# Kernel optimization log

Hardware: AMD Instinct MI355X
Metric: run time of the kernel (lower is better)

## Reference

```python
import jax, jax.numpy as jnp
import numpy as np

N_CHANNELS = 512
D_K = 64
N_HEADS = N_CHANNELS // D_K  # 8
SCALE = 1.0 / np.sqrt(np.sqrt(D_K))
EPS = 1e-8


def pixnorm(x, axis=-1):
    return x * jax.lax.rsqrt(jnp.mean(x * x, axis=axis, keepdims=True) + EPS)


def setup_inputs() -> dict:
    key = jax.random.key(0)
    k1, k2, k3 = jax.random.split(key, 3)
    x = jax.random.normal(k1, (16, N_CHANNELS, 32, 32), dtype=jnp.float32)
    # 1x1 conv weights (bias=False) stored as [out, in]
    w_proj = jax.random.normal(k2, (3 * N_CHANNELS, N_CHANNELS), dtype=jnp.float32) * (1.0 / np.sqrt(N_CHANNELS))
    w_out = jax.random.normal(k3, (N_CHANNELS, N_CHANNELS), dtype=jnp.float32) * (1.0 / np.sqrt(N_CHANNELS))
    return {"x": x, "w_proj": w_proj, "w_out": w_out}


def reference(x, w_proj, w_out):
    B, C, H, W = x.shape
    S = H * W
    # tokens: [B, S, C]
    xt = x.reshape(B, C, S).transpose(0, 2, 1)
    # 1x1 conv projection -> [B, S, 3C]
    h = jnp.einsum('bsc,oc->bso', xt, w_proj)
    qkv = h.reshape(B, S, N_HEADS, 3 * D_K)
    q, k, v = jnp.split(qkv, 3, axis=-1)  # each [B, S, H, d]
    q = pixnorm(q)
    k = pixnorm(k)
    v = pixnorm(v)
    attn = jnp.einsum('bihd,bjhd->bijh', q * SCALE, k * SCALE)
    attn = jax.nn.softmax(attn, axis=2)
    res = jnp.einsum('bijh,bjhd->bihd', attn, v)  # [B, S, H, d]
    res = res.reshape(B, S, C)
    res = jnp.einsum('bsc,oc->bso', res, w_out)
    res = res.transpose(0, 2, 1).reshape(B, C, H, W)
    return x + res
```

## Files before the change

kernel.cpp:

```cpp
#include <hip/hip_runtime.h>
#include <hip/hip_bf16.h>
#include <math.h>

typedef float f32x4 __attribute__((ext_vector_type(4)));
typedef __bf16 bf16x8 __attribute__((ext_vector_type(8)));
typedef __bf16 bf16x4 __attribute__((ext_vector_type(4)));
typedef unsigned u32x4 __attribute__((ext_vector_type(4)));

#define DEVFN static __device__ __forceinline__

DEVFN void gload16(const void* g, void* l) {
  __builtin_amdgcn_global_load_lds(
      (const __attribute__((address_space(1))) unsigned int*)g,
      (__attribute__((address_space(3))) unsigned int*)l, 16, 0, 0);
}

DEVFN f32x4 mfma16(bf16x8 a, bf16x8 b, f32x4 c) {
  return __builtin_amdgcn_mfma_f32_16x16x32_bf16(a, b, c, 0, 0, 0);
}

DEVFN unsigned cvtpk(float lo, float hi) {
  unsigned r;
  asm("v_cvt_pk_bf16_f32 %0, %1, %2" : "=v"(r) : "v"(lo), "v"(hi));
  return r;
}

#define WAITV4() asm volatile("s_waitcnt vmcnt(4)" ::: "memory")
#define WAITV0() asm volatile("s_waitcnt vmcnt(0)" ::: "memory")

__global__ __launch_bounds__(256) void cast_weights_k(
    const float* __restrict__ wp, const float* __restrict__ wo,
    __bf16* __restrict__ wpb, __bf16* __restrict__ wob) {
  int i = blockIdx.x * 256 + threadIdx.x;
  if (i < 1536 * 512) {
    wpb[i] = (__bf16)wp[i];
  } else {
    int j = i - 1536 * 512;
    wob[j] = (__bf16)wo[j];
  }
}

__global__ __launch_bounds__(256) void transpose_x_k(const float* __restrict__ x,
                                                     __bf16* __restrict__ xt) {
  __shared__ float tile[64][65];
  int b = blockIdx.z, c0 = blockIdx.y * 64, s0 = blockIdx.x * 64;
  int t = threadIdx.x;
  int r = t >> 2, q = (t & 3) << 4;
  const float* src = x + ((size_t)(b * 512 + c0 + r)) * 1024 + s0 + q;
#pragma unroll
  for (int i = 0; i < 4; i++) {
    float4 f = *reinterpret_cast<const float4*>(src + i * 4);
    tile[r][q + i * 4 + 0] = f.x;
    tile[r][q + i * 4 + 1] = f.y;
    tile[r][q + i * 4 + 2] = f.z;
    tile[r][q + i * 4 + 3] = f.w;
  }
  __syncthreads();
  bf16x8 o0, o1;
#pragma unroll
  for (int i = 0; i < 8; i++) o0[i] = (__bf16)tile[q + i][r];
#pragma unroll
  for (int i = 0; i < 8; i++) o1[i] = (__bf16)tile[q + 8 + i][r];
  __bf16* dst = xt + ((size_t)(b * 1024 + s0 + r)) * 512 + c0 + q;
  *reinterpret_cast<bf16x8*>(dst) = o0;
  *reinterpret_cast<bf16x8*>(dst + 8) = o1;
}

template <int MODE>
__global__ __launch_bounds__(256, 4) void gemm_bt_k(
    const __bf16* __restrict__ A, const __bf16* __restrict__ Bt,
    float* __restrict__ Cf, const float* __restrict__ Xres,
    __bf16* __restrict__ Qo, __bf16* __restrict__ Ko, __bf16* __restrict__ Vto) {
  __shared__ __attribute__((aligned(16))) char smem[32768];
  const int K = 512;
  int p = blockIdx.x, xcd = p & 7, idx = p >> 3;
  int m0, n0, z;
  if (MODE == 2) {
    m0 = (xcd * 16 + idx / 12) * 128;
    n0 = (idx % 12) * 128;
    z = 0;
  } else {
    z = xcd * 2 + idx / 32;
    int rem = idx % 32;
    m0 = (rem >> 3) * 128;
    n0 = (rem & 7) * 128;
    Bt += (size_t)z * (1024L * 512);
  }
  int tid = threadIdx.x, wave = tid >> 6, lane = tid & 63;
  int fr = lane & 15, fq = lane >> 4;
  int wm = (wave >> 1) * 64, wn = (wave & 1) * 64;
  f32x4 acc[4][4] = {};
  int offs[2], rr[2], scc[2];
#pragma unroll
  for (int i = 0; i < 2; i++) {
    offs[i] = wave * 2048 + i * 1024 + lane * 16;
    rr[i] = offs[i] >> 6;
    scc[i] = (offs[i] & 63) ^ (((rr[i] ^ (rr[i] >> 2)) & 3) << 4);
  }
  int rdsw = (fr ^ (fr >> 2)) & 3;
  const char* Ap = (const char*)A;
  const char* Bp = (const char*)Bt;

#define GSTAGE(k0_, buf_)                                                       \
  {                                                                             \
    char* as_ = smem + (buf_)*8192;                                             \
    char* bs_ = smem + 16384 + (buf_)*8192;                                     \
    _Pragma("unroll") for (int i = 0; i < 2; i++)                               \
        gload16(Ap + (size_t)(m0 + rr[i]) * 1024 + (k0_)*2 + scc[i],            \
                as_ + offs[i]);                                                 \
    _Pragma("unroll") for (int i = 0; i < 2; i++)                               \
        gload16(Bp + (size_t)(n0 + rr[i]) * 1024 + (k0_)*2 + scc[i],            \
                bs_ + offs[i]);                                                 \
  }

  GSTAGE(0, 0);
  GSTAGE(32, 1);
  int cur = 0;
  for (int k0 = 0; k0 < K; k0 += 32) {
    if (k0 + 32 < K) WAITV4(); else WAITV0();
    __builtin_amdgcn_s_barrier();
    __builtin_amdgcn_sched_barrier(0);
    const char* as = smem + cur * 8192;
    const char* bs = smem + 16384 + cur * 8192;
    bf16x8 af[4], bfr[4];
#pragma unroll
    for (int mi = 0; mi < 4; mi++)
      af[mi] = *reinterpret_cast<const bf16x8*>(
          as + (wm + mi * 16 + fr) * 64 + ((fq ^ rdsw) << 4));
#pragma unroll
    for (int ni = 0; ni < 4; ni++)
      bfr[ni] = *reinterpret_cast<const bf16x8*>(
          bs + (wn + ni * 16 + fr) * 64 + ((fq ^ rdsw) << 4));
    __builtin_amdgcn_s_setprio(1);
#pragma unroll
    for (int mi = 0; mi < 4; mi++)
#pragma unroll
      for (int ni = 0; ni < 4; ni++)
        acc[mi][ni] = mfma16(af[mi], bfr[ni], acc[mi][ni]);
    __builtin_amdgcn_s_setprio(0);
    __builtin_amdgcn_s_barrier();
    if (k0 + 64 < K) GSTAGE(k0 + 64, cur);
    cur ^= 1;
  }
#undef GSTAGE

  if (MODE == 1) {
    float* Co = Cf + (size_t)z * (512L * 1024);
    const float* Xr = Xres + (size_t)z * (512L * 1024);
#pragma unroll
    for (int mi = 0; mi < 4; mi++)
#pragma unroll
      for (int i = 0; i < 4; i++) {
        int row = m0 + wm + mi * 16 + fq * 4 + i;
#pragma unroll
        for (int ni = 0; ni < 4; ni++) {
          size_t idxo = (size_t)row * 1024 + n0 + wn + ni * 16 + fr;
          Co[idxo] = acc[mi][ni][i] + Xr[idxo];
        }
      }
  } else {
    int g0 = n0 + wn;
    int head = g0 / 192;
    int grp = (g0 >> 6) % 3;
    int b = m0 >> 10, sb = m0 & 1023;
    int bh = b * 8 + head;
    float nrm[4][4];
#pragma unroll
    for (int mi = 0; mi < 4; mi++)
#pragma unroll
      for (int i = 0; i < 4; i++) {
        float ss = 0.f;
#pragma unroll
        for (int ni = 0; ni < 4; ni++) ss += acc[mi][ni][i] * acc[mi][ni][i];
#pragma unroll
        for (int off = 1; off < 16; off <<= 1) ss += __shfl_xor(ss, off);
        float nv = rsqrtf(ss * (1.0f / 64.0f) + 1e-8f);
        if (grp == 0) nv *= 0.18033688011112042f;
        nrm[mi][i] = nv;
      }
    if (grp < 2) {
      __bf16* dst = (grp == 0 ? Qo : Ko) + (size_t)bh * 65536;
#pragma unroll
      for (int mi = 0; mi < 4; mi++)
#pragma unroll
        for (int i = 0; i < 4; i++) {
          int s = sb + wm + mi * 16 + fq * 4 + i;
#pragma unroll
          for (int ni = 0; ni < 4; ni++)
            dst[(size_t)s * 64 + ni * 16 + fr] = (__bf16)(acc[mi][ni][i] * nrm[mi][i]);
        }
    }
    __syncthreads();
    if (grp == 2) {
#pragma unroll
      for (int mi = 0; mi < 4; mi++)
#pragma unroll
        for (int i = 0; i < 4; i++) {
          int r = wm + mi * 16 + fq * 4 + i;
#pragma unroll
          for (int ni = 0; ni < 4; ni++) {
            int col2 = (2 * (ni * 16 + fr)) ^ ((r & 31) << 2);
            *(__bf16*)(smem + r * 128 + col2) = (__bf16)(acc[mi][ni][i] * nrm[mi][i]);
          }
        }
    }
    __syncthreads();
    if (grp == 2) {
      int sl = wm + lane;
      int l = sl & 63;
      int pl = ((l >> 2) & 3) * 16 + (l >> 4) * 4 + (l & 3);
      __bf16* vdst = Vto + (size_t)bh * 65536 + sb + (sl & 64) + pl;
#pragma unroll 8
      for (int d = 0; d < 64; d++) {
        __bf16 v = *(const __bf16*)(smem + sl * 128 + ((2 * d) ^ ((sl & 31) << 2)));
        vdst[(size_t)d * 1024] = v;
      }
    }
  }
}

__global__ __launch_bounds__(256, 4) void attn_k(const __bf16* __restrict__ Q,
                                                 const __bf16* __restrict__ Kb,
                                                 const __bf16* __restrict__ Vt,
                                                 __bf16* __restrict__ Res) {
  __shared__ __attribute__((aligned(16))) char lds[32768];
  int p = blockIdx.x;
  int v = (p & 7) * 128 + (p >> 3);
  int qt = v & 7, bh = v >> 3;
  int wave = threadIdx.x >> 6, lane = threadIdx.x & 63;
  int fr = lane & 15, fq = lane >> 4;
  const __bf16* Qb = Q + (size_t)bh * 65536;
  const char* Kbase = (const char*)(Kb + (size_t)bh * 65536);
  const char* Vbase = (const char*)(Vt + (size_t)bh * 65536);
  bf16x8 qf[2][2];
#pragma unroll
  for (int qs = 0; qs < 2; qs++)
#pragma unroll
    for (int kk = 0; kk < 2; kk++)
      qf[qs][kk] = *reinterpret_cast<const bf16x8*>(
          Qb + (size_t)(qt * 128 + qs * 64 + wave * 16 + fr) * 64 + kk * 32 + fq * 8);

  bf16x8 ones;
#pragma unroll
  for (int j = 0; j < 8; j++) ones[j] = (__bf16)1.0f;

  f32x4 oa[2][4] = {};
  f32x4 lacc[2] = {};

  int o0 = wave * 2048 + lane * 16;
  int o1 = o0 + 1024;
  int r0 = o0 >> 7, c0 = o0 & 127, r1 = o1 >> 7, c1 = o1 & 127;
  int s0 = c0 ^ ((r0 & 7) << 4), s1 = c1 ^ ((r1 & 7) << 4);
  int swr = (fr & 7) << 4;

#define STAGE(kt_, buf_)                                                        \
  {                                                                             \
    char* ks_ = lds + (buf_)*8192;                                              \
    char* vs_ = lds + 16384 + (buf_)*8192;                                      \
    gload16(Kbase + (size_t)(kt_)*8192 + r0 * 128 + s0, ks_ + o0);              \
    gload16(Kbase + (size_t)(kt_)*8192 + r1 * 128 + s1, ks_ + o1);              \
    gload16(Vbase + (size_t)r0 * 2048 + (kt_)*128 + s0, vs_ + o0);              \
    gload16(Vbase + (size_t)r1 * 2048 + (kt_)*128 + s1, vs_ + o1);              \
  }

#define QKT(buf_)                                                               \
  {                                                                             \
    const char* ksc_ = lds + (buf_)*8192;                                       \
    __builtin_amdgcn_s_setprio(1);                                              \
    _Pragma("unroll") for (int ni = 0; ni < 4; ni++) {                          \
      bf16x8 kf0 = *reinterpret_cast<const bf16x8*>(                            \
          ksc_ + (ni * 16 + fr) * 128 + ((fq * 16) ^ swr));                     \
      bf16x8 kf1 = *reinterpret_cast<const bf16x8*>(                            \
          ksc_ + (ni * 16 + fr) * 128 + ((64 + fq * 16) ^ swr));                \
      _Pragma("unroll") for (int qs = 0; qs < 2; qs++) {                        \
        sa[qs][ni] = mfma16(kf0, qf[qs][0], sa[qs][ni]);                        \
        sa[qs][ni] = mfma16(kf1, qf[qs][1], sa[qs][ni]);                        \
      }                                                                         \
    }                                                                           \
    __builtin_amdgcn_s_setprio(0);                                              \
  }

  STAGE(0, 0);
  STAGE(1, 1);
  WAITV4();
  __builtin_amdgcn_s_barrier();
  __builtin_amdgcn_sched_barrier(0);
  f32x4 sa[2][4] = {};
  QKT(0);
  for (int kt = 0; kt < 16; kt++) {
    int cur = kt & 1;
    const char* vsc = lds + 16384 + cur * 8192;
    bf16x8 pb[2][2];
#pragma unroll
    for (int qs = 0; qs < 2; qs++) {
#pragma unroll
      for (int ni = 0; ni < 4; ni++)
#pragma unroll
        for (int i = 0; i < 4; i++)
          sa[qs][ni][i] = __builtin_amdgcn_exp2f(sa[qs][ni][i]);
#pragma unroll
      for (int kk2 = 0; kk2 < 2; kk2++) {
        u32x4 u;
        u[0] = cvtpk(sa[qs][2 * kk2][0], sa[qs][2 * kk2][1]);
        u[1] = cvtpk(sa[qs][2 * kk2][2], sa[qs][2 * kk2][3]);
        u[2] = cvtpk(sa[qs][2 * kk2 + 1][0], sa[qs][2 * kk2 + 1][1]);
        u[3] = cvtpk(sa[qs][2 * kk2 + 1][2], sa[qs][2 * kk2 + 1][3]);
        pb[qs][kk2] = __builtin_bit_cast(bf16x8, u);
      }
      lacc[qs] = mfma16(ones, pb[qs][0], lacc[qs]);
      lacc[qs] = mfma16(ones, pb[qs][1], lacc[qs]);
    }
    __builtin_amdgcn_s_setprio(1);
#pragma unroll
    for (int nd = 0; nd < 4; nd++) {
      int vrow = (nd * 16 + fr) * 128;
#pragma unroll
      for (int kk2 = 0; kk2 < 2; kk2++) {
        bf16x8 vf = *reinterpret_cast<const bf16x8*>(
            vsc + vrow + ((fq * 32 + kk2 * 16) ^ swr));
#pragma unroll
        for (int qs = 0; qs < 2; qs++)
          oa[qs][nd] = mfma16(vf, pb[qs][kk2], oa[qs][nd]);
      }
    }
    __builtin_amdgcn_s_setprio(0);
    if (kt == 15) break;
    __builtin_amdgcn_s_barrier();
    if (kt + 2 < 16) {
      STAGE(kt + 2, cur);
      WAITV4();
    } else {
      WAITV0();
    }
    __builtin_amdgcn_s_barrier();
    __builtin_amdgcn_sched_barrier(0);
#pragma unroll
    for (int qs = 0; qs < 2; qs++)
#pragma unroll
      for (int ni = 0; ni < 4; ni++) sa[qs][ni] = (f32x4){0.f, 0.f, 0.f, 0.f};
    QKT(cur ^ 1);
  }
  int b = bh >> 3, hd = bh & 7;
#pragma unroll
  for (int qs = 0; qs < 2; qs++) {
    int q = qt * 128 + qs * 64 + wave * 16 + fr;
    float inv_l = 1.0f / lacc[qs][0];
    __bf16* dst = Res + ((size_t)(b * 1024 + q)) * 512 + hd * 64 + fq * 4;
#pragma unroll
    for (int nd = 0; nd < 4; nd++) {
      bf16x4 ov;
#pragma unroll
      for (int i = 0; i < 4; i++) ov[i] = (__bf16)(oa[qs][nd][i] * inv_l);
      *reinterpret_cast<bf16x4*>(dst + nd * 16) = ov;
    }
  }
#undef STAGE
#undef QKT
}

extern "C" void kernel_launch(void* const* d_in, const int* in_sizes, int n_in,
                              void* d_out, int out_size, void* d_ws, size_t ws_size,
                              hipStream_t stream) {
  const float* x = (const float*)d_in[0];
  const float* wp = (const float*)d_in[1];
  const float* wo = (const float*)d_in[2];
  float* out = (float*)d_out;
  char* w = (char*)d_ws;
  __bf16* wpb = (__bf16*)(w);
  __bf16* wob = (__bf16*)(w + 1572864);
  __bf16* xt = (__bf16*)(w + 2097152);
  __bf16* Qb = (__bf16*)(w + 18874368);
  __bf16* Kb = (__bf16*)(w + 35651584);
  __bf16* Vtb = (__bf16*)(w + 52428800);
  __bf16* resb = (__bf16*)(w + 69206016);

  cast_weights_k<<<4096, 256, 0, stream>>>(wp, wo, wpb, wob);
  transpose_x_k<<<dim3(16, 8, 16), 256, 0, stream>>>(x, xt);
  gemm_bt_k<2><<<1536, 256, 0, stream>>>(xt, wpb, nullptr, nullptr, Qb, Kb, Vtb);
  attn_k<<<1024, 256, 0, stream>>>(Qb, Kb, Vtb, resb);
  gemm_bt_k<1><<<512, 256, 0, stream>>>(wob, resb, out, x, nullptr, nullptr,
                                        nullptr);
}
```

Baseline: 118.7 us.

## Restructure GEMM to 256x64 tiles with LDS-resident B and register-streamed A

Changes GEMM block tiles from 128x128 to 256x64. The whole 64xK B slice is loaded into 64KB LDS once up front, and A fragments are read directly from global memory into registers with double buffering. This removes the per-k-step barriers and the LDS staging of A. In exchange, LDS use rises to 64KB per block, which reduces occupancy, and A is read straight from global/L2 without any staging. The V-transpose epilogue is adjusted so each block handles a single q/k/v group.

After: 154.6 us. 1.3x slower.

```diff
diff --git a/kernel.cpp b/kernel.cpp
--- a/kernel.cpp
+++ b/kernel.cpp
@@ -67,82 +67,67 @@
 }
 
 template <int MODE>
-__global__ __launch_bounds__(256, 4) void gemm_bt_k(
+__global__ __launch_bounds__(256) void gemm_bt_k(
     const __bf16* __restrict__ A, const __bf16* __restrict__ Bt,
     float* __restrict__ Cf, const float* __restrict__ Xres,
     __bf16* __restrict__ Qo, __bf16* __restrict__ Ko, __bf16* __restrict__ Vto) {
-  __shared__ __attribute__((aligned(16))) char smem[32768];
-  const int K = 512;
+  __shared__ __attribute__((aligned(16))) char smem[65536];
   int p = blockIdx.x, xcd = p & 7, idx = p >> 3;
   int m0, n0, z;
   if (MODE == 2) {
-    m0 = (xcd * 16 + idx / 12) * 128;
-    n0 = (idx % 12) * 128;
+    m0 = (xcd * 8 + idx / 24) * 256;
+    n0 = (idx % 24) * 64;
     z = 0;
   } else {
     z = xcd * 2 + idx / 32;
     int rem = idx % 32;
-    m0 = (rem >> 3) * 128;
-    n0 = (rem & 7) * 128;
+    m0 = (rem >> 4) * 256;
+    n0 = (rem & 15) * 64;
     Bt += (size_t)z * (1024L * 512);
   }
   int tid = threadIdx.x, wave = tid >> 6, lane = tid & 63;
   int fr = lane & 15, fq = lane >> 4;
-  int wm = (wave >> 1) * 64, wn = (wave & 1) * 64;
+
+  {
+    int srow = tid >> 2, sslot = tid & 3;
+    int ssw = (srow ^ (srow >> 2)) & 3;
+    const char* Bsrc = (const char*)Bt + (size_t)(n0 + srow) * 1024 +
+                       ((sslot ^ ssw) << 4);
+#pragma unroll
+    for (int j = 0; j < 16; j++)
+      gload16(Bsrc + j * 64, smem + j * 4096 + tid * 16);
+  }
+  __syncthreads();
+
+  const char* Abase = (const char*)A + (size_t)(m0 + wave * 64 + fr) * 1024 + fq * 16;
+  int rdsw4 = ((fr ^ (fr >> 2)) & 3) << 4;
   f32x4 acc[4][4] = {};
-  int offs[2], rr[2], scc[2];
-#pragma unroll
-  for (int i = 0; i < 2; i++) {
-    offs[i] = wave * 2048 + i * 1024 + lane * 16;
-    rr[i] = offs[i] >> 6;
-    scc[i] = (offs[i] & 63) ^ (((rr[i] ^ (rr[i] >> 2)) & 3) << 4);
-  }
-  int rdsw = (fr ^ (fr >> 2)) & 3;
-  const char* Ap = (const char*)A;
-  const char* Bp = (const char*)Bt;
-
-#define GSTAGE(k0_, buf_)                                                       \
-  {                                                                             \
-    char* as_ = smem + (buf_)*8192;                                             \
-    char* bs_ = smem + 16384 + (buf_)*8192;                                     \
-    _Pragma("unroll") for (int i = 0; i < 2; i++)                               \
-        gload16(Ap + (size_t)(m0 + rr[i]) * 1024 + (k0_)*2 + scc[i],            \
-                as_ + offs[i]);                                                 \
-    _Pragma("unroll") for (int i = 0; i < 2; i++)                               \
-        gload16(Bp + (size_t)(n0 + rr[i]) * 1024 + (k0_)*2 + scc[i],            \
-                bs_ + offs[i]);                                                 \
-  }
-
-  GSTAGE(0, 0);
-  GSTAGE(32, 1);
-  int cur = 0;
-  for (int k0 = 0; k0 < K; k0 += 32) {
-    if (k0 + 32 < K) WAITV4(); else WAITV0();
-    __builtin_amdgcn_s_barrier();
-    __builtin_amdgcn_sched_barrier(0);
-    const char* as = smem + cur * 8192;
-    const char* bs = smem + 16384 + cur * 8192;
-    bf16x8 af[4], bfr[4];
-#pragma unroll
-    for (int mi = 0; mi < 4; mi++)
-      af[mi] = *reinterpret_cast<const bf16x8*>(
-          as + (wm + mi * 16 + fr) * 64 + ((fq ^ rdsw) << 4));
+  bf16x8 af[2][4];
+#pragma unroll
+  for (int mi = 0; mi < 4; mi++)
+    af[0][mi] = *reinterpret_cast<const bf16x8*>(Abase + mi * 16384);
+
+#pragma unroll
+  for (int kt = 0; kt < 16; kt++) {
+    if (kt + 1 < 16) {
+#pragma unroll
+      for (int mi = 0; mi < 4; mi++)
+        af[(kt + 1) & 1][mi] = *reinterpret_cast<const bf16x8*>(
+            Abase + mi * 16384 + (kt + 1) * 64);
+    }
+    bf16x8 bfr[4];
 #pragma unroll
     for (int ni = 0; ni < 4; ni++)
       bfr[ni] = *reinterpret_cast<const bf16x8*>(
-          bs + (wn + ni * 16 + fr) * 64 + ((fq ^ rdsw) << 4));
+          smem + kt * 4096 + (ni * 16 + fr) * 64 + ((fq << 4) ^ rdsw4));
     __builtin_amdgcn_s_setprio(1);
 #pragma unroll
     for (int mi = 0; mi < 4; mi++)
 #pragma unroll
       for (int ni = 0; ni < 4; ni++)
-        acc[mi][ni] = mfma16(af[mi], bfr[ni], acc[mi][ni]);
+        acc[mi][ni] = mfma16(af[kt & 1][mi], bfr[ni], acc[mi][ni]);
     __builtin_amdgcn_s_setprio(0);
-    __builtin_amdgcn_s_barrier();
-    if (k0 + 64 < K) GSTAGE(k0 + 64, cur);
-    cur ^= 1;
-  }
-#undef GSTAGE
+  }
 
   if (MODE == 1) {
     float* Co = Cf + (size_t)z * (512L * 1024);
@@ -151,17 +136,16 @@
     for (int mi = 0; mi < 4; mi++)
 #pragma unroll
       for (int i = 0; i < 4; i++) {
-        int row = m0 + wm + mi * 16 + fq * 4 + i;
+        int row = m0 + wave * 64 + mi * 16 + fq * 4 + i;
 #pragma unroll
         for (int ni = 0; ni < 4; ni++) {
-          size_t idxo = (size_t)row * 1024 + n0 + wn + ni * 16 + fr;
+          size_t idxo = (size_t)row * 1024 + n0 + ni * 16 + fr;
           Co[idxo] = acc[mi][ni][i] + Xr[idxo];
         }
       }
   } else {
-    int g0 = n0 + wn;
-    int head = g0 / 192;
-    int grp = (g0 >> 6) % 3;
+    int head = n0 / 192;
+    int grp = (n0 >> 6) % 3;
     int b = m0 >> 10, sb = m0 & 1023;
     int bh = b * 8 + head;
     float nrm[4][4];
@@ -184,36 +168,32 @@
       for (int mi = 0; mi < 4; mi++)
 #pragma unroll
         for (int i = 0; i < 4; i++) {
-          int s = sb + wm + mi * 16 + fq * 4 + i;
+          int s = sb + wave * 64 + mi * 16 + fq * 4 + i;
 #pragma unroll
           for (int ni = 0; ni < 4; ni++)
             dst[(size_t)s * 64 + ni * 16 + fr] = (__bf16)(acc[mi][ni][i] * nrm[mi][i]);
         }
-    }
-    __syncthreads();
-    if (grp == 2) {
+    } else {
+      __syncthreads();
 #pragma unroll
       for (int mi = 0; mi < 4; mi++)
 #pragma unroll
         for (int i = 0; i < 4; i++) {
-          int r = wm + mi * 16 + fq * 4 + i;
+          int r = wave * 64 + mi * 16 + fq * 4 + i;
 #pragma unroll
           for (int ni = 0; ni < 4; ni++) {
             int col2 = (2 * (ni * 16 + fr)) ^ ((r & 31) << 2);
             *(__bf16*)(smem + r * 128 + col2) = (__bf16)(acc[mi][ni][i] * nrm[mi][i]);
           }
         }
-    }
-    __syncthreads();
-    if (grp == 2) {
-      int sl = wm + lane;
-      int l = sl & 63;
+      __syncthreads();
+      int l = tid & 63;
       int pl = ((l >> 2) & 3) * 16 + (l >> 4) * 4 + (l & 3);
-      __bf16* vdst = Vto + (size_t)bh * 65536 + sb + (sl & 64) + pl;
+      __bf16* vdst = Vto + (size_t)bh * 65536 + sb + (tid & 192) + pl;
 #pragma unroll 8
       for (int d = 0; d < 64; d++) {
-        __bf16 v = *(const __bf16*)(smem + sl * 128 + ((2 * d) ^ ((sl & 31) << 2)));
-        vdst[(size_t)d * 1024] = v;
+        __bf16 vv = *(const __bf16*)(smem + tid * 128 + ((2 * d) ^ ((tid & 31) << 2)));
+        vdst[(size_t)d * 1024] = vv;
       }
     }
   }
```

## Use 256x256-tile 512-thread QKV projection GEMM with 128-deep K stages

Applied to the files above, without the earlier changes.

Splits the templated GEMM into a dedicated QKV projection kernel and an output-projection kernel. The QKV kernel uses 256x256 output tiles, 8 waves and 128-wide K stages double-buffered in 128KB of LDS, which cuts the number of global loads per FLOP and the number of barriers. This trades occupancy (one block per CU, 384 blocks on 256 CUs) and much higher register pressure for better data reuse. The pixnorm and V-transpose epilogue is adapted to per-wave 128x64 tiles.

New measurement: 129.1 us. 8.8% more time.

```diff
diff --git a/kernel.cpp b/kernel.cpp
--- a/kernel.cpp
+++ b/kernel.cpp
@@ -25,6 +25,7 @@
   return r;
 }
 
+#define WAITV8() asm volatile("s_waitcnt vmcnt(8)" ::: "memory")
 #define WAITV4() asm volatile("s_waitcnt vmcnt(4)" ::: "memory")
 #define WAITV0() asm volatile("s_waitcnt vmcnt(0)" ::: "memory")
 
@@ -66,26 +67,165 @@
   *reinterpret_cast<bf16x8*>(dst + 8) = o1;
 }
 
-template <int MODE>
-__global__ __launch_bounds__(256, 4) void gemm_bt_k(
+__global__ __launch_bounds__(512) void gemm_qkv_k(
     const __bf16* __restrict__ A, const __bf16* __restrict__ Bt,
-    float* __restrict__ Cf, const float* __restrict__ Xres,
     __bf16* __restrict__ Qo, __bf16* __restrict__ Ko, __bf16* __restrict__ Vto) {
+  __shared__ __attribute__((aligned(16))) char smem[131072];
+  int p = blockIdx.x, xcd = p & 7, idx = p >> 3;
+  int m0 = (xcd * 8 + idx / 6) * 256;
+  int n0 = (idx % 6) * 256;
+  int tid = threadIdx.x, wave = tid >> 6, lane = tid & 63;
+  int fr = lane & 15, fq = lane >> 4;
+  int wr = wave >> 2, wc = wave & 3;
+  const char* Ap = (const char*)A;
+  const char* Bp = (const char*)Bt;
+  int so[2], srow[2], ssw[2];
+#pragma unroll
+  for (int j = 0; j < 2; j++) {
+    so[j] = j * 8192 + tid * 16;
+    srow[j] = so[j] >> 7;
+    ssw[j] = (so[j] & 127) ^ ((srow[j] & 7) << 4);
+  }
+  int swr = (fr & 7) << 4;
+
+#define GSTAGE(kt_, buf_)                                                       \
+  {                                                                             \
+    char* ab_ = smem + (buf_)*32768;                                            \
+    char* bb_ = smem + 65536 + (buf_)*32768;                                    \
+    _Pragma("unroll") for (int h = 0; h < 2; h++)                               \
+        _Pragma("unroll") for (int j = 0; j < 2; j++) {                         \
+      gload16(Ap + (size_t)(m0 + h * 128 + srow[j]) * 1024 + (kt_)*128 + ssw[j],\
+              ab_ + h * 16384 + so[j]);                                         \
+      gload16(Bp + (size_t)(n0 + h * 128 + srow[j]) * 1024 + (kt_)*128 + ssw[j],\
+              bb_ + h * 16384 + so[j]);                                         \
+    }                                                                           \
+  }
+
+  f32x4 acc[8][4] = {};
+  GSTAGE(0, 0);
+  GSTAGE(1, 1);
+#pragma unroll
+  for (int kt = 0; kt < 8; kt++) {
+    if (kt < 7) WAITV8(); else WAITV0();
+    __builtin_amdgcn_s_barrier();
+    __builtin_amdgcn_sched_barrier(0);
+    const char* ab = smem + (kt & 1) * 32768 + wr * 16384;
+    const char* bb = smem + 65536 + (kt & 1) * 32768;
+#pragma unroll
+    for (int mh = 0; mh < 2; mh++) {
+      bf16x8 af[4][2];
+#pragma unroll
+      for (int m4 = 0; m4 < 4; m4++) {
+        int rloc = (mh * 4 + m4) * 16 + fr;
+#pragma unroll
+        for (int kk = 0; kk < 2; kk++)
+          af[m4][kk] = *reinterpret_cast<const bf16x8*>(
+              ab + rloc * 128 + ((kk * 64 + fq * 16) ^ swr));
+      }
+#pragma unroll
+      for (int nh = 0; nh < 2; nh++) {
+        bf16x8 bfr[2][2];
+#pragma unroll
+        for (int n2 = 0; n2 < 2; n2++) {
+          int rn = wc * 64 + (nh * 2 + n2) * 16 + fr;
+#pragma unroll
+          for (int kk = 0; kk < 2; kk++)
+            bfr[n2][kk] = *reinterpret_cast<const bf16x8*>(
+                bb + (rn >> 7) * 16384 + (rn & 127) * 128 +
+                ((kk * 64 + fq * 16) ^ swr));
+        }
+        __builtin_amdgcn_s_setprio(1);
+#pragma unroll
+        for (int m4 = 0; m4 < 4; m4++)
+#pragma unroll
+          for (int n2 = 0; n2 < 2; n2++)
+#pragma unroll
+            for (int kk = 0; kk < 2; kk++)
+              acc[mh * 4 + m4][nh * 2 + n2] =
+                  mfma16(af[m4][kk], bfr[n2][kk], acc[mh * 4 + m4][nh * 2 + n2]);
+        __builtin_amdgcn_s_setprio(0);
+      }
+    }
+    __builtin_amdgcn_s_barrier();
+    if (kt + 2 < 8) GSTAGE(kt + 2, kt & 1);
+  }
+#undef GSTAGE
+
+  int gi = (n0 >> 6) + wc;
+  int head = gi / 3;
+  int grp = gi % 3;
+  int b = m0 >> 10, sb = m0 & 1023;
+  int bh = b * 8 + head;
+  float nrm[8][4];
+#pragma unroll
+  for (int mi = 0; mi < 8; mi++)
+#pragma unroll
+    for (int i = 0; i < 4; i++) {
+      float ss = 0.f;
+#pragma unroll
+      for (int ni = 0; ni < 4; ni++) ss += acc[mi][ni][i] * acc[mi][ni][i];
+#pragma unroll
+      for (int off = 1; off < 16; off <<= 1) ss += __shfl_xor(ss, off);
+      float nv = rsqrtf(ss * (1.0f / 64.0f) + 1e-8f);
+      if (grp == 0) nv *= 0.18033688011112042f;
+      nrm[mi][i] = nv;
+    }
+  if (grp < 2) {
+    __bf16* dst = (grp == 0 ? Qo : Ko) + (size_t)bh * 65536;
+#pragma unroll
+    for (int mi = 0; mi < 8; mi++)
+#pragma unroll
+      for (int i = 0; i < 4; i++) {
+        int s = sb + wr * 128 + mi * 16 + fq * 4 + i;
+#pragma unroll
+        for (int ni = 0; ni < 4; ni++)
+          dst[(size_t)s * 64 + ni * 16 + fr] = (__bf16)(acc[mi][ni][i] * nrm[mi][i]);
+      }
+  }
+  __syncthreads();
+  if (grp == 2) {
+    char* wb = smem + wave * 16384;
+#pragma unroll
+    for (int mi = 0; mi < 8; mi++)
+#pragma unroll
+      for (int i = 0; i < 4; i++) {
+        int r = mi * 16 + fq * 4 + i;
+#pragma unroll
+        for (int ni = 0; ni < 4; ni++) {
+          int col2 = (2 * (ni * 16 + fr)) ^ ((r & 31) << 2);
+          *(__bf16*)(wb + r * 128 + col2) = (__bf16)(acc[mi][ni][i] * nrm[mi][i]);
+        }
+      }
+  }
+  __syncthreads();
+  if (grp == 2) {
+    const char* wb = smem + wave * 16384;
+    int pl = ((lane >> 2) & 3) * 16 + (lane >> 4) * 4 + (lane & 3);
+#pragma unroll
+    for (int rep = 0; rep < 2; rep++) {
+      int row = rep * 64 + lane;
+      int base64 = sb + wr * 128 + rep * 64;
+      __bf16* vdst = Vto + (size_t)bh * 65536 + base64 + pl;
+#pragma unroll 8
+      for (int d = 0; d < 64; d++) {
+        __bf16 vv = *(const __bf16*)(wb + row * 128 + ((2 * d) ^ ((row & 31) << 2)));
+        vdst[(size_t)d * 1024] = vv;
+      }
+    }
+  }
+}
+
+__global__ __launch_bounds__(256, 4) void gemm_out_k(
+    const __bf16* __restrict__ A, const __bf16* __restrict__ Bt,
+    float* __restrict__ Cf, const float* __restrict__ Xres) {
   __shared__ __attribute__((aligned(16))) char smem[32768];
   const int K = 512;
   int p = blockIdx.x, xcd = p & 7, idx = p >> 3;
-  int m0, n0, z;
-  if (MODE == 2) {
-    m0 = (xcd * 16 + idx / 12) * 128;
-    n0 = (idx % 12) * 128;
-    z = 0;
-  } else {
-    z = xcd * 2 + idx / 32;
-    int rem = idx % 32;
-    m0 = (rem >> 3) * 128;
-    n0 = (rem & 7) * 128;
-    Bt += (size_t)z * (1024L * 512);
-  }
+  int z = xcd * 2 + idx / 32;
+  int rem = idx % 32;
+  int m0 = (rem >> 3) * 128;
+  int n0 = (rem & 7) * 128;
+  Bt += (size_t)z * (1024L * 512);
   int tid = threadIdx.x, wave = tid >> 6, lane = tid & 63;
   int fr = lane & 15, fq = lane >> 4;
   int wm = (wave >> 1) * 64, wn = (wave & 1) * 64;
@@ -144,79 +284,19 @@
   }
 #undef GSTAGE
 
-  if (MODE == 1) {
-    float* Co = Cf + (size_t)z * (512L * 1024);
-    const float* Xr = Xres + (size_t)z * (512L * 1024);
-#pragma unroll
-    for (int mi = 0; mi < 4; mi++)
-#pragma unroll
-      for (int i = 0; i < 4; i++) {
-        int row = m0 + wm + mi * 16 + fq * 4 + i;
-#pragma unroll
-        for (int ni = 0; ni < 4; ni++) {
-          size_t idxo = (size_t)row * 1024 + n0 + wn + ni * 16 + fr;
-          Co[idxo] = acc[mi][ni][i] + Xr[idxo];
-        }
-      }
-  } else {
-    int g0 = n0 + wn;
-    int head = g0 / 192;
-    int grp = (g0 >> 6) % 3;
-    int b = m0 >> 10, sb = m0 & 1023;
-    int bh = b * 8 + head;
-    float nrm[4][4];
-#pragma unroll
-    for (int mi = 0; mi < 4; mi++)
-#pragma unroll
-      for (int i = 0; i < 4; i++) {
-        float ss = 0.f;
-#pragma unroll
-        for (int ni = 0; ni < 4; ni++) ss += acc[mi][ni][i] * acc[mi][ni][i];
-#pragma unroll
-        for (int off = 1; off < 16; off <<= 1) ss += __shfl_xor(ss, off);
-        float nv = rsqrtf(ss * (1.0f / 64.0f) + 1e-8f);
-        if (grp == 0) nv *= 0.18033688011112042f;
-        nrm[mi][i] = nv;
-      }
-    if (grp < 2) {
-      __bf16* dst = (grp == 0 ? Qo : Ko) + (size_t)bh * 65536;
-#pragma unroll
-      for (int mi = 0; mi < 4; mi++)
-#pragma unroll
-        for (int i = 0; i < 4; i++) {
-          int s = sb + wm + mi * 16 + fq * 4 + i;
-#pragma unroll
-          for (int ni = 0; ni < 4; ni++)
-            dst[(size_t)s * 64 + ni * 16 + fr] = (__bf16)(acc[mi][ni][i] * nrm[mi][i]);
-        }
-    }
-    __syncthreads();
-    if (grp == 2) {
-#pragma unroll
-      for (int mi = 0; mi < 4; mi++)
-#pragma unroll
-        for (int i = 0; i < 4; i++) {
-          int r = wm + mi * 16 + fq * 4 + i;
-#pragma unroll
-          for (int ni = 0; ni < 4; ni++) {
-            int col2 = (2 * (ni * 16 + fr)) ^ ((r & 31) << 2);
-            *(__bf16*)(smem + r * 128 + col2) = (__bf16)(acc[mi][ni][i] * nrm[mi][i]);
-          }
-        }
-    }
-    __syncthreads();
-    if (grp == 2) {
-      int sl = wm + lane;
-      int l = sl & 63;
-      int pl = ((l >> 2) & 3) * 16 + (l >> 4) * 4 + (l & 3);
-      __bf16* vdst = Vto + (size_t)bh * 65536 + sb + (sl & 64) + pl;
-#pragma unroll 8
-      for (int d = 0; d < 64; d++) {
-        __bf16 v = *(const __bf16*)(smem + sl * 128 + ((2 * d) ^ ((sl & 31) << 2)));
-        vdst[(size_t)d * 1024] = v;
-      }
-    }
-  }
+  float* Co = Cf + (size_t)z * (512L * 1024);
+  const float* Xr = Xres + (size_t)z * (512L * 1024);
+#pragma unroll
+  for (int mi = 0; mi < 4; mi++)
+#pragma unroll
+    for (int i = 0; i < 4; i++) {
+      int row = m0 + wm + mi * 16 + fq * 4 + i;
+#pragma unroll
+      for (int ni = 0; ni < 4; ni++) {
+        size_t idxo = (size_t)row * 1024 + n0 + wn + ni * 16 + fr;
+        Co[idxo] = acc[mi][ni][i] + Xr[idxo];
+      }
+    }
 }
 
 __global__ __launch_bounds__(256, 4) void attn_k(const __bf16* __restrict__ Q,
@@ -376,8 +456,7 @@
 
   cast_weights_k<<<4096, 256, 0, stream>>>(wp, wo, wpb, wob);
   transpose_x_k<<<dim3(16, 8, 16), 256, 0, stream>>>(x, xt);
-  gemm_bt_k<2><<<1536, 256, 0, stream>>>(xt, wpb, nullptr, nullptr, Qb, Kb, Vtb);
+  gemm_qkv_k<<<384, 512, 0, stream>>>(xt, wpb, Qb, Kb, Vtb);
   attn_k<<<1024, 256, 0, stream>>>(Qb, Kb, Vtb, resb);
-  gemm_bt_k<1><<<512, 256, 0, stream>>>(wob, resb, out, x, nullptr, nullptr,
-                                        nullptr);
-}
+  gemm_out_k<<<512, 256, 0, stream>>>(wob, resb, out, x);
+}
```

## Fuse weight cast into transpose kernel and triple-buffer GEMM K loop

Applied to the files above, without the earlier changes.

The standalone weight-cast kernel is merged into the x-transpose kernel, so each block also converts 512 weight elements, which removes one kernel launch. The GEMM main loop moves from a double-buffered LDS ring to a triple-buffered one. The prefetch for stage t+2 is issued right after the fragment reads, which drops the second barrier per iteration and fully unrolls the loop. LDS per block grows from 32KB to 48KB, which may lower occupancy below the launch_bounds target of 4 blocks per CU.

Measured after the change: 116.9 us. No clear change (-1.5%).

```diff
diff --git a/kernel.cpp b/kernel.cpp
--- a/kernel.cpp
+++ b/kernel.cpp
@@ -28,20 +28,10 @@
 #define WAITV4() asm volatile("s_waitcnt vmcnt(4)" ::: "memory")
 #define WAITV0() asm volatile("s_waitcnt vmcnt(0)" ::: "memory")
 
-__global__ __launch_bounds__(256) void cast_weights_k(
+__global__ __launch_bounds__(256) void transpose_x_k(
+    const float* __restrict__ x, __bf16* __restrict__ xt,
     const float* __restrict__ wp, const float* __restrict__ wo,
     __bf16* __restrict__ wpb, __bf16* __restrict__ wob) {
-  int i = blockIdx.x * 256 + threadIdx.x;
-  if (i < 1536 * 512) {
-    wpb[i] = (__bf16)wp[i];
-  } else {
-    int j = i - 1536 * 512;
-    wob[j] = (__bf16)wo[j];
-  }
-}
-
-__global__ __launch_bounds__(256) void transpose_x_k(const float* __restrict__ x,
-                                                     __bf16* __restrict__ xt) {
   __shared__ float tile[64][65];
   int b = blockIdx.z, c0 = blockIdx.y * 64, s0 = blockIdx.x * 64;
   int t = threadIdx.x;
@@ -55,6 +45,18 @@
     tile[r][q + i * 4 + 2] = f.z;
     tile[r][q + i * 4 + 3] = f.w;
   }
+  int lid = (blockIdx.z * 8 + blockIdx.y) * 16 + blockIdx.x;
+  int wi = lid * 512 + t * 2;
+  if (wi < 786432) {
+    float2 f = *reinterpret_cast<const float2*>(wp + wi);
+    wpb[wi] = (__bf16)f.x;
+    wpb[wi + 1] = (__bf16)f.y;
+  } else {
+    int j = wi - 786432;
+    float2 f = *reinterpret_cast<const float2*>(wo + j);
+    wob[j] = (__bf16)f.x;
+    wob[j + 1] = (__bf16)f.y;
+  }
   __syncthreads();
   bf16x8 o0, o1;
 #pragma unroll
@@ -71,8 +73,7 @@
     const __bf16* __restrict__ A, const __bf16* __restrict__ Bt,
     float* __restrict__ Cf, const float* __restrict__ Xres,
     __bf16* __restrict__ Qo, __bf16* __restrict__ Ko, __bf16* __restrict__ Vto) {
-  __shared__ __attribute__((aligned(16))) char smem[32768];
-  const int K = 512;
+  __shared__ __attribute__((aligned(16))) char smem[49152];
   int p = blockIdx.x, xcd = p & 7, idx = p >> 3;
   int m0, n0, z;
   if (MODE == 2) {
@@ -101,10 +102,10 @@
   const char* Ap = (const char*)A;
   const char* Bp = (const char*)Bt;
 
-#define GSTAGE(k0_, buf_)                                                       \
+#define GSTAGE(k0_, slot_)                                                      \
   {                                                                             \
-    char* as_ = smem + (buf_)*8192;                                             \
-    char* bs_ = smem + 16384 + (buf_)*8192;                                     \
+    char* as_ = smem + (slot_)*16384;                                           \
+    char* bs_ = as_ + 8192;                                                     \
     _Pragma("unroll") for (int i = 0; i < 2; i++)                               \
         gload16(Ap + (size_t)(m0 + rr[i]) * 1024 + (k0_)*2 + scc[i],            \
                 as_ + offs[i]);                                                 \
@@ -115,13 +116,13 @@
 
   GSTAGE(0, 0);
   GSTAGE(32, 1);
-  int cur = 0;
-  for (int k0 = 0; k0 < K; k0 += 32) {
-    if (k0 + 32 < K) WAITV4(); else WAITV0();
+#pragma unroll
+  for (int t = 0; t < 16; t++) {
+    if (t < 15) WAITV4(); else WAITV0();
     __builtin_amdgcn_s_barrier();
     __builtin_amdgcn_sched_barrier(0);
-    const char* as = smem + cur * 8192;
-    const char* bs = smem + 16384 + cur * 8192;
+    const char* as = smem + (t % 3) * 16384;
+    const char* bs = as + 8192;
     bf16x8 af[4], bfr[4];
 #pragma unroll
     for (int mi = 0; mi < 4; mi++)
@@ -131,6 +132,7 @@
     for (int ni = 0; ni < 4; ni++)
       bfr[ni] = *reinterpret_cast<const bf16x8*>(
           bs + (wn + ni * 16 + fr) * 64 + ((fq ^ rdsw) << 4));
+    if (t + 2 < 16) GSTAGE((t + 2) * 32, (t + 2) % 3);
     __builtin_amdgcn_s_setprio(1);
 #pragma unroll
     for (int mi = 0; mi < 4; mi++)
@@ -138,9 +140,6 @@
       for (int ni = 0; ni < 4; ni++)
         acc[mi][ni] = mfma16(af[mi], bfr[ni], acc[mi][ni]);
     __builtin_amdgcn_s_setprio(0);
-    __builtin_amdgcn_s_barrier();
-    if (k0 + 64 < K) GSTAGE(k0 + 64, cur);
-    cur ^= 1;
   }
 #undef GSTAGE
 
@@ -374,8 +373,7 @@
   __bf16* Vtb = (__bf16*)(w + 52428800);
   __bf16* resb = (__bf16*)(w + 69206016);
 
-  cast_weights_k<<<4096, 256, 0, stream>>>(wp, wo, wpb, wob);
-  transpose_x_k<<<dim3(16, 8, 16), 256, 0, stream>>>(x, xt);
+  transpose_x_k<<<dim3(16, 8, 16), 256, 0, stream>>>(x, xt, wp, wo, wpb, wob);
   gemm_bt_k<2><<<1536, 256, 0, stream>>>(xt, wpb, nullptr, nullptr, Qb, Kb, Vtb);
   attn_k<<<1024, 256, 0, stream>>>(Qb, Kb, Vtb, resb);
   gemm_bt_k<1><<<512, 256, 0, stream>>>(wob, resb, out, x, nullptr, nullptr,
```
